# Kernel tuning notes

Measured on AMD Instinct MI355X. Metric: run time of the kernel, lower is better.

The kernel has to match this reference:

```python
import jax, jax.numpy as jnp
import numpy as np

N = 50000
E = 800000
F = 128


def gcn_smooth(edge_index, x):
    """Symmetric-normalized GCN smoothing: D^-1/2 (A + I) D^-1/2 x.

    edge_index: [2, E] int (src, dst) of a sparse graph; self-loops added here.
    x: [N, F] float node features.
    """
    src, dst = edge_index[0], edge_index[1]
    n = x.shape[0]
    # degree of A + I
    deg = jax.ops.segment_sum(jnp.ones((src.shape[0],), x.dtype), dst, num_segments=n) + 1.0
    dinv = jax.lax.rsqrt(deg)  # [N]
    # per-edge normalization d^-1/2[src] * d^-1/2[dst]
    norm_e = dinv[src] * dinv[dst]  # [E]
    msg = x[src] * norm_e[:, None]  # [E, F] -- gather + scale
    agg = jax.ops.segment_sum(msg, dst, num_segments=n)  # scatter-add over dst
    # self-loop contribution: dinv[i]^2 * x[i]
    return agg + (dinv * dinv)[:, None] * x


def setup_inputs() -> dict:
    key = jax.random.key(0)
    ks = jax.random.split(key, 12)
    inp = {
        "X_HypGNet": jax.random.normal(ks[0], (N, F), jnp.float32),
        "X_CGNet": jax.random.normal(ks[1], (N, F), jnp.float32),
        "X_SGNet": jax.random.normal(ks[2], (N, F), jnp.float32),
        "edge_index_hyp": jax.random.randint(ks[3], (2, E), 0, N, dtype=jnp.int32),
        "edge_index_c": jax.random.randint(ks[4], (2, E), 0, N, dtype=jnp.int32),
        "edge_index_s": jax.random.randint(ks[5], (2, E), 0, N, dtype=jnp.int32),
        "W_hyp": jax.random.normal(ks[6], (F, F), jnp.float32) * 0.05,
        "b_hyp": jax.random.normal(ks[7], (F,), jnp.float32) * 0.05,
        "W_cg": jax.random.normal(ks[8], (F, F), jnp.float32) * 0.05,
        "b_cg": jax.random.normal(ks[9], (F,), jnp.float32) * 0.05,
        "W_sg": jax.random.normal(ks[10], (F, F), jnp.float32) * 0.05,
        "b_sg": jax.random.normal(ks[11], (F,), jnp.float32) * 0.05,
    }
    return inp


def reference(X_HypGNet, X_CGNet, X_SGNet, edge_index_hyp, edge_index_c, edge_index_s,
              W_hyp, b_hyp, W_cg, b_cg, W_sg, b_sg):
    X_hyp = X_HypGNet @ W_hyp + b_hyp
    X_cg = X_CGNet @ W_cg + b_cg
    X_sg = X_SGNet @ W_sg + b_sg
    X_hyp_s = gcn_smooth(edge_index_hyp, X_hyp)
    X_cg_s = gcn_smooth(edge_index_c, X_cg)
    X_sg_s = gcn_smooth(edge_index_s, X_sg)
    return (X_hyp_s, X_cg_s, X_sg_s)
```

## Files before the change

### kernel.cpp

```cpp
#include <hip/hip_runtime.h>

#define F_DIM 128
#define NG 3
#define AEPT 16
#define CAP 48
#define MAXBIN 256
#define SPILL_CAP 8192

typedef __attribute__((ext_vector_type(8))) short short8_t;
typedef __attribute__((ext_vector_type(4))) float f32x4;

__device__ __forceinline__ unsigned short f2bf(float f) {
    unsigned int x = __float_as_uint(f);
    unsigned int r = x + 0x7fffu + ((x >> 16) & 1u);
    return (unsigned short)(r >> 16);
}
__device__ __forceinline__ float bflo(unsigned int u) { return __uint_as_float(u << 16); }
__device__ __forceinline__ float bfhi(unsigned int u) { return __uint_as_float(u & 0xffff0000u); }

struct GArgs {
    const int* src[NG]; const int* dst[NG];
    const float* X[NG]; const float* W[NG]; const float* b[NG];
    float* out[NG];
    unsigned short* Xps[NG];
    unsigned short* sorted[NG];
    int* binbuf[NG];
    int* bincur[NG];
    int* cstore[NG];
    float* dinv[NG];
    int* spill[NG];
    int* spill_n[NG];
    int nbin, bincap;
};

__global__ __launch_bounds__(256) void init_kernel(GArgs a, int g0) {
    int g = g0 + blockIdx.y;
    for (int i = threadIdx.x; i < a.nbin; i += 256) a.bincur[g][i] = i * a.bincap;
    if (threadIdx.x == 0) a.spill_n[g][0] = 0;
}

__global__ __launch_bounds__(256) void binA_kernel(GArgs a, int g0, int E) {
    int g = g0 + blockIdx.y;
    __shared__ int cnt[MAXBIN];
    __shared__ int lcur[MAXBIN];
    const int t = threadIdx.x;
    const int nbin = a.nbin, bincap = a.bincap;
    for (int i = t; i < nbin; i += 256) cnt[i] = 0;
    __syncthreads();
    const int* dst = a.dst[g];
    const int* src = a.src[g];
    const int base = blockIdx.x * (256 * AEPT) + t;
    int dd[AEPT], sv[AEPT];
#pragma unroll
    for (int i = 0; i < AEPT; ++i) {
        int e = base + i * 256;
        int ec = (e < E) ? e : 0;
        dd[i] = __builtin_nontemporal_load(&dst[ec]);
        sv[i] = __builtin_nontemporal_load(&src[ec]);
        if (e < E) atomicAdd(&cnt[dd[i] >> 8], 1);
    }
    __syncthreads();
    for (int i = t; i < nbin; i += 256) {
        int c = cnt[i];
        lcur[i] = c ? atomicAdd(&a.bincur[g][i], c) : 0;
    }
    __syncthreads();
    int* binbuf = a.binbuf[g];
#pragma unroll
    for (int i = 0; i < AEPT; ++i) {
        int e = base + i * 256;
        if (e < E) {
            int bin = dd[i] >> 8;
            int pos = atomicAdd(&lcur[bin], 1);
            if (pos < (bin + 1) * bincap) {
                binbuf[pos] = ((dd[i] & 255) << 16) | sv[i];
            } else {
                int sp = atomicAdd(a.spill_n[g], 1);
                if (sp < SPILL_CAP) {
                    a.spill[g][2 * sp] = sv[i];
                    a.spill[g][2 * sp + 1] = dd[i];
                }
            }
        }
    }
}

__global__ __launch_bounds__(256) void binB_kernel(GArgs a, int g0, int n) {
    int g = g0 + blockIdx.y;
    int bin = blockIdx.x;
    const int t = threadIdx.x;
    __shared__ int cnt[256];
    cnt[t] = 0;
    __syncthreads();
    const int bincap = a.bincap;
    int used = a.bincur[g][bin] - bin * bincap;
    int rd = min(used, bincap);
    const int* bb = a.binbuf[g] + bin * bincap;
    unsigned short* sorted = a.sorted[g];
    for (int j = t; j < rd; j += 256) {
        int u = bb[j];
        int dl = u >> 16;
        int s = u & 0xffff;
        int tk = atomicAdd(&cnt[dl], 1);
        int d = (bin << 8) + dl;
        if (tk < CAP) {
            sorted[d * CAP + tk] = (unsigned short)s;
        } else {
            int sp = atomicAdd(a.spill_n[g], 1);
            if (sp < SPILL_CAP) {
                a.spill[g][2 * sp] = s;
                a.spill[g][2 * sp + 1] = d;
            }
        }
    }
    __syncthreads();
    int d = (bin << 8) + t;
    if (d < n) {
        int deg = cnt[t];
        a.cstore[g][d] = min(deg, CAP);
        a.dinv[g][d] = rsqrtf((float)deg + 1.0f);
    }
}

__global__ __launch_bounds__(256) void gemm_kernel(GArgs a, int g0, int n) {
    int g = g0 + blockIdx.y;
    __shared__ unsigned short Xl[128 * 128];
    __shared__ unsigned short Wt[128 * 128];
    const int t = threadIdx.x;
    const int row0 = blockIdx.x * 128;
    const float* X = a.X[g];
    const float* W = a.W[g];
    char* XlB = (char*)Xl;
    char* WtB = (char*)Wt;

    for (int i = t; i < 128 * 16; i += 256) {
        int r = i >> 4, kc = i & 15;
        int row = row0 + r;
        float4 x0 = make_float4(0.f, 0.f, 0.f, 0.f), x1 = x0;
        if (row < n) {
            const float4* xp = (const float4*)(X + (size_t)row * F_DIM + kc * 8);
            x0 = xp[0]; x1 = xp[1];
        }
        uint4 pk;
        pk.x = (unsigned)f2bf(x0.x) | ((unsigned)f2bf(x0.y) << 16);
        pk.y = (unsigned)f2bf(x0.z) | ((unsigned)f2bf(x0.w) << 16);
        pk.z = (unsigned)f2bf(x1.x) | ((unsigned)f2bf(x1.y) << 16);
        pk.w = (unsigned)f2bf(x1.z) | ((unsigned)f2bf(x1.w) << 16);
        unsigned int ad = (unsigned)((r << 8) + (kc << 4)) ^ (unsigned)((r & 15) << 4);
        *(uint4*)(XlB + ad) = pk;
    }
    for (int i = t; i < 128 * 16; i += 256) {
        int nn = i & 127, kc = i >> 7;
        const float* wp = W + (size_t)(kc * 8) * F_DIM + nn;
        uint4 pk;
        pk.x = (unsigned)f2bf(wp[0])   | ((unsigned)f2bf(wp[128]) << 16);
        pk.y = (unsigned)f2bf(wp[256]) | ((unsigned)f2bf(wp[384]) << 16);
        pk.z = (unsigned)f2bf(wp[512]) | ((unsigned)f2bf(wp[640]) << 16);
        pk.w = (unsigned)f2bf(wp[768]) | ((unsigned)f2bf(wp[896]) << 16);
        unsigned int ad = (unsigned)((nn << 8) + (kc << 4)) ^ (unsigned)((nn & 15) << 4);
        *(uint4*)(WtB + ad) = pk;
    }
    __syncthreads();

    const int l = t & 63;
    const int wv = t >> 6;
    const int wr = wv >> 1, wc = wv & 1;
    const int lm = l & 15;
    const int lk = l >> 4;

    f32x4 acc[4][4] = {};
#pragma unroll
    for (int ks = 0; ks < 4; ++ks) {
        const int kb = ks * 64 + lk * 16;
        short8_t af[4], bv[4];
#pragma unroll
        for (int mt = 0; mt < 4; ++mt) {
            int r = wr * 64 + mt * 16 + lm;
            unsigned int ad = (unsigned)((r << 8) + kb) ^ (unsigned)((r & 15) << 4);
            af[mt] = *(const short8_t*)(XlB + ad);
        }
#pragma unroll
        for (int nt = 0; nt < 4; ++nt) {
            int c = wc * 64 + nt * 16 + lm;
            unsigned int ad = (unsigned)((c << 8) + kb) ^ (unsigned)((c & 15) << 4);
            bv[nt] = *(const short8_t*)(WtB + ad);
        }
#pragma unroll
        for (int mt = 0; mt < 4; ++mt)
#pragma unroll
            for (int nt = 0; nt < 4; ++nt)
                acc[mt][nt] = __builtin_amdgcn_mfma_f32_16x16x32_bf16(af[mt], bv[nt],
                                                                      acc[mt][nt], 0, 0, 0);
    }

    const float* bia = a.b[g];
    const float* dinv = a.dinv[g];
    unsigned short* Xps = a.Xps[g];
#pragma unroll
    for (int nt = 0; nt < 4; ++nt) {
        int col = wc * 64 + nt * 16 + lm;
        float bc = bia[col];
#pragma unroll
        for (int mt = 0; mt < 4; ++mt) {
            int rbase = row0 + wr * 64 + mt * 16 + lk * 4;
#pragma unroll
            for (int r = 0; r < 4; ++r) {
                int row = rbase + r;
                if (row < n) {
                    float v = (acc[mt][nt][r] + bc) * dinv[row];
                    Xps[(size_t)row * F_DIM + col] = f2bf(v);
                }
            }
        }
    }
}

__global__ __launch_bounds__(256) void agg_kernel(GArgs a, int g, int n) {
    int wave = (blockIdx.x * 256 + threadIdx.x) >> 6;
    if (wave >= n) return;
    const int l = threadIdx.x & 63;
    const int c = l & 15;
    const int hi = l >> 4;
    const uint4* Xp4 = (const uint4*)a.Xps[g];
    const unsigned short* sorted = a.sorted[g];
    int cnt = a.cstore[g][wave];
    int s = (l < cnt) ? (int)__builtin_nontemporal_load(&sorted[(size_t)wave * CAP + l]) : 0;
    float a0 = 0.f, a1 = 0.f, a2 = 0.f, a3 = 0.f, a4 = 0.f, a5 = 0.f, a6 = 0.f, a7 = 0.f;
    for (int k = 0; k < cnt; k += 8) {
        int e0 = k + hi, e1 = k + 4 + hi;
        int s0 = __shfl(s, e0, 64);
        int s1 = __shfl(s, e1 < 48 ? e1 : 0, 64);
        uint4 v0 = Xp4[(size_t)s0 * 16 + c];
        uint4 v1 = Xp4[(size_t)s1 * 16 + c];
        if (e0 >= cnt) v0 = make_uint4(0u, 0u, 0u, 0u);
        if (e1 >= cnt) v1 = make_uint4(0u, 0u, 0u, 0u);
        a0 += bflo(v0.x); a1 += bfhi(v0.x);
        a2 += bflo(v0.y); a3 += bfhi(v0.y);
        a4 += bflo(v0.z); a5 += bfhi(v0.z);
        a6 += bflo(v0.w); a7 += bfhi(v0.w);
        a0 += bflo(v1.x); a1 += bfhi(v1.x);
        a2 += bflo(v1.y); a3 += bfhi(v1.y);
        a4 += bflo(v1.z); a5 += bfhi(v1.z);
        a6 += bflo(v1.w); a7 += bfhi(v1.w);
    }
    a0 += __shfl_xor(a0, 16, 64); a0 += __shfl_xor(a0, 32, 64);
    a1 += __shfl_xor(a1, 16, 64); a1 += __shfl_xor(a1, 32, 64);
    a2 += __shfl_xor(a2, 16, 64); a2 += __shfl_xor(a2, 32, 64);
    a3 += __shfl_xor(a3, 16, 64); a3 += __shfl_xor(a3, 32, 64);
    a4 += __shfl_xor(a4, 16, 64); a4 += __shfl_xor(a4, 32, 64);
    a5 += __shfl_xor(a5, 16, 64); a5 += __shfl_xor(a5, 32, 64);
    a6 += __shfl_xor(a6, 16, 64); a6 += __shfl_xor(a6, 32, 64);
    a7 += __shfl_xor(a7, 16, 64); a7 += __shfl_xor(a7, 32, 64);
    uint4 v = Xp4[(size_t)wave * 16 + c];
    a0 += bflo(v.x); a1 += bfhi(v.x);
    a2 += bflo(v.y); a3 += bfhi(v.y);
    a4 += bflo(v.z); a5 += bfhi(v.z);
    a6 += bflo(v.w); a7 += bfhi(v.w);
    float dd = a.dinv[g][wave];
    if (hi == 0) {
        float* o = (float*)a.out[g] + (size_t)wave * F_DIM + c * 8;
        *(float4*)(o + 0) = make_float4(a0 * dd, a1 * dd, a2 * dd, a3 * dd);
        *(float4*)(o + 4) = make_float4(a4 * dd, a5 * dd, a6 * dd, a7 * dd);
    }
}

__global__ __launch_bounds__(128) void spill_kernel(GArgs a, int g0) {
    int g = g0 + blockIdx.y;
    int ns = min(a.spill_n[g][0], SPILL_CAP);
    const unsigned short* Xps = a.Xps[g];
    const float* dinv = a.dinv[g];
    float* out = a.out[g];
    for (int i = blockIdx.x; i < ns; i += gridDim.x) {
        int s = a.spill[g][2 * i];
        int d = a.spill[g][2 * i + 1];
        float w = dinv[d];
        int f = threadIdx.x;
        float v = __uint_as_float(((unsigned int)Xps[(size_t)s * F_DIM + f]) << 16);
        unsafeAtomicAdd(&out[(size_t)d * F_DIM + f], w * v);
    }
}

extern "C" void kernel_launch(void* const* d_in, const int* in_sizes, int n_in,
                              void* d_out, int out_size, void* d_ws, size_t ws_size,
                              hipStream_t stream) {
    const float* Xin[NG] = {(const float*)d_in[0], (const float*)d_in[1], (const float*)d_in[2]};
    const int* ei[NG] = {(const int*)d_in[3], (const int*)d_in[4], (const int*)d_in[5]};
    const float* Wk[NG] = {(const float*)d_in[6], (const float*)d_in[8], (const float*)d_in[10]};
    const float* bk[NG] = {(const float*)d_in[7], (const float*)d_in[9], (const float*)d_in[11]};

    const int N = in_sizes[0] / F_DIM;
    const int E = in_sizes[3] / 2;
    float* out = (float*)d_out;

    const int nbin = (N + 255) >> 8;
    const int bincap = E / nbin + E / (3 * nbin) + 256;

    const size_t xps_b = (size_t)N * F_DIM * 2;
    const size_t sorted_b = (size_t)N * CAP * 2;
    const size_t binbuf_b = (size_t)nbin * bincap * 4;
    const size_t nb = (size_t)N * 4;
    const size_t bincur_b = ((size_t)nbin * 4 + 255) / 256 * 256;
    const size_t spill_b = (size_t)SPILL_CAP * 8 + 64;
    const size_t per = ((xps_b + sorted_b + binbuf_b + 2 * nb + bincur_b + spill_b + 255)
                        / 256) * 256;
    const bool fused = ws_size >= (size_t)NG * per;
    char* base = (char*)d_ws;

    GArgs a;
    a.nbin = nbin;
    a.bincap = bincap;
    for (int r = 0; r < NG; ++r) {
        char* s = base + (size_t)(fused ? r : 0) * per;
        size_t off = 0;
        a.Xps[r] = (unsigned short*)(s + off); off += xps_b;
        a.sorted[r] = (unsigned short*)(s + off); off += sorted_b;
        a.binbuf[r] = (int*)(s + off); off += binbuf_b;
        a.cstore[r] = (int*)(s + off); off += nb;
        a.dinv[r] = (float*)(s + off); off += nb;
        a.bincur[r] = (int*)(s + off); off += bincur_b;
        a.spill[r] = (int*)(s + off);
        a.spill_n[r] = (int*)(s + off + spill_b - 64);
        a.src[r] = ei[r];
        a.dst[r] = ei[r] + E;
        a.X[r] = Xin[r];
        a.W[r] = Wk[r];
        a.b[r] = bk[r];
        a.out[r] = out + (size_t)r * N * F_DIM;
    }

    const dim3 blk(256);
    const int gAe = (E + 256 * AEPT - 1) / (256 * AEPT);
    const int gR = (N + 127) / 128;
    const int gG = (N * 64 + 255) / 256;

    if (fused) {
        init_kernel<<<dim3(1, NG), blk, 0, stream>>>(a, 0);
        binA_kernel<<<dim3(gAe, NG), blk, 0, stream>>>(a, 0, E);
        binB_kernel<<<dim3(nbin, NG), blk, 0, stream>>>(a, 0, N);
        gemm_kernel<<<dim3(gR, NG), blk, 0, stream>>>(a, 0, N);
        for (int g = 0; g < NG; ++g)
            agg_kernel<<<dim3(gG, 1), blk, 0, stream>>>(a, g, N);
        spill_kernel<<<dim3(16, NG), dim3(128), 0, stream>>>(a, 0);
    } else {
        for (int g = 0; g < NG; ++g) {
            init_kernel<<<dim3(1, 1), blk, 0, stream>>>(a, g);
            binA_kernel<<<dim3(gAe, 1), blk, 0, stream>>>(a, g, E);
            binB_kernel<<<dim3(nbin, 1), blk, 0, stream>>>(a, g, N);
            gemm_kernel<<<dim3(gR, 1), blk, 0, stream>>>(a, g, N);
            agg_kernel<<<dim3(gG, 1), blk, 0, stream>>>(a, g, N);
            spill_kernel<<<dim3(16, 1), dim3(128), 0, stream>>>(a, g);
        }
    }
}
```

Before: 201.6 us.

## Pre-convert weights once and load GEMM operands directly into registers

A new small kernel converts each W to bf16 in MFMA fragment layout once per graph. The GEMM then drops its LDS staging and barrier, loading X rows straight from global memory into registers and converting them to bf16 in place. The three per-graph aggregation launches are merged into one launch indexed by blockIdx.y. This removes per-block redundant W conversion, LDS traffic and launch overhead, but X loads are no longer coalesced through shared memory and an extra kernel launch is added.

After: 193.0 us. -4.3%, faster.

```diff
diff --git a/kernel.cpp b/kernel.cpp
--- a/kernel.cpp
+++ b/kernel.cpp
@@ -18,12 +18,22 @@
 __device__ __forceinline__ float bflo(unsigned int u) { return __uint_as_float(u << 16); }
 __device__ __forceinline__ float bfhi(unsigned int u) { return __uint_as_float(u & 0xffff0000u); }
 
+__device__ __forceinline__ short8_t cvt8(float4 x0, float4 x1) {
+    union { short8_t s; uint4 u; } pk;
+    pk.u.x = (unsigned)f2bf(x0.x) | ((unsigned)f2bf(x0.y) << 16);
+    pk.u.y = (unsigned)f2bf(x0.z) | ((unsigned)f2bf(x0.w) << 16);
+    pk.u.z = (unsigned)f2bf(x1.x) | ((unsigned)f2bf(x1.y) << 16);
+    pk.u.w = (unsigned)f2bf(x1.z) | ((unsigned)f2bf(x1.w) << 16);
+    return pk.s;
+}
+
 struct GArgs {
     const int* src[NG]; const int* dst[NG];
     const float* X[NG]; const float* W[NG]; const float* b[NG];
     float* out[NG];
     unsigned short* Xps[NG];
     unsigned short* sorted[NG];
+    unsigned short* Wtb[NG];
     int* binbuf[NG];
     int* bincur[NG];
     int* cstore[NG];
@@ -37,6 +47,22 @@
     int g = g0 + blockIdx.y;
     for (int i = threadIdx.x; i < a.nbin; i += 256) a.bincur[g][i] = i * a.bincap;
     if (threadIdx.x == 0) a.spill_n[g][0] = 0;
+}
+
+__global__ __launch_bounds__(256) void prew_kernel(GArgs a, int g0) {
+    int g = g0 + blockIdx.y;
+    const float* W = a.W[g];
+    unsigned short* Wtb = a.Wtb[g];
+    for (int i = threadIdx.x; i < 16 * 128; i += 256) {
+        int kg = i >> 7, c = i & 127;
+        const float* wp = W + (size_t)(kg * 8) * F_DIM + c;
+        uint4 pk;
+        pk.x = (unsigned)f2bf(wp[0])   | ((unsigned)f2bf(wp[128]) << 16);
+        pk.y = (unsigned)f2bf(wp[256]) | ((unsigned)f2bf(wp[384]) << 16);
+        pk.z = (unsigned)f2bf(wp[512]) | ((unsigned)f2bf(wp[640]) << 16);
+        pk.w = (unsigned)f2bf(wp[768]) | ((unsigned)f2bf(wp[896]) << 16);
+        *(uint4*)(Wtb + (size_t)i * 8) = pk;
+    }
 }
 
 __global__ __launch_bounds__(256) void binA_kernel(GArgs a, int g0, int E) {
@@ -124,85 +150,54 @@
 
 __global__ __launch_bounds__(256) void gemm_kernel(GArgs a, int g0, int n) {
     int g = g0 + blockIdx.y;
-    __shared__ unsigned short Xl[128 * 128];
-    __shared__ unsigned short Wt[128 * 128];
     const int t = threadIdx.x;
-    const int row0 = blockIdx.x * 128;
-    const float* X = a.X[g];
-    const float* W = a.W[g];
-    char* XlB = (char*)Xl;
-    char* WtB = (char*)Wt;
-
-    for (int i = t; i < 128 * 16; i += 256) {
-        int r = i >> 4, kc = i & 15;
-        int row = row0 + r;
-        float4 x0 = make_float4(0.f, 0.f, 0.f, 0.f), x1 = x0;
-        if (row < n) {
-            const float4* xp = (const float4*)(X + (size_t)row * F_DIM + kc * 8);
-            x0 = xp[0]; x1 = xp[1];
-        }
-        uint4 pk;
-        pk.x = (unsigned)f2bf(x0.x) | ((unsigned)f2bf(x0.y) << 16);
-        pk.y = (unsigned)f2bf(x0.z) | ((unsigned)f2bf(x0.w) << 16);
-        pk.z = (unsigned)f2bf(x1.x) | ((unsigned)f2bf(x1.y) << 16);
-        pk.w = (unsigned)f2bf(x1.z) | ((unsigned)f2bf(x1.w) << 16);
-        unsigned int ad = (unsigned)((r << 8) + (kc << 4)) ^ (unsigned)((r & 15) << 4);
-        *(uint4*)(XlB + ad) = pk;
-    }
-    for (int i = t; i < 128 * 16; i += 256) {
-        int nn = i & 127, kc = i >> 7;
-        const float* wp = W + (size_t)(kc * 8) * F_DIM + nn;
-        uint4 pk;
-        pk.x = (unsigned)f2bf(wp[0])   | ((unsigned)f2bf(wp[128]) << 16);
-        pk.y = (unsigned)f2bf(wp[256]) | ((unsigned)f2bf(wp[384]) << 16);
-        pk.z = (unsigned)f2bf(wp[512]) | ((unsigned)f2bf(wp[640]) << 16);
-        pk.w = (unsigned)f2bf(wp[768]) | ((unsigned)f2bf(wp[896]) << 16);
-        unsigned int ad = (unsigned)((nn << 8) + (kc << 4)) ^ (unsigned)((nn & 15) << 4);
-        *(uint4*)(WtB + ad) = pk;
-    }
-    __syncthreads();
-
     const int l = t & 63;
     const int wv = t >> 6;
     const int wr = wv >> 1, wc = wv & 1;
-    const int lm = l & 15;
-    const int lk = l >> 4;
+    const int lm = l & 15, lk = l >> 4;
+    const int rowA = blockIdx.x * 128 + wr * 64 + lm;
+    const float* X = a.X[g];
+    const unsigned short* Wtb = a.Wtb[g];
 
     f32x4 acc[4][4] = {};
 #pragma unroll
     for (int ks = 0; ks < 4; ++ks) {
-        const int kb = ks * 64 + lk * 16;
-        short8_t af[4], bv[4];
+        short8_t bv[4];
+#pragma unroll
+        for (int nt = 0; nt < 4; ++nt) {
+            int col = wc * 64 + nt * 16 + lm;
+            bv[nt] = *(const short8_t*)(Wtb + ((size_t)((ks * 4 + lk) * 128 + col)) * 8);
+        }
+        float4 xr[4][2];
 #pragma unroll
         for (int mt = 0; mt < 4; ++mt) {
-            int r = wr * 64 + mt * 16 + lm;
-            unsigned int ad = (unsigned)((r << 8) + kb) ^ (unsigned)((r & 15) << 4);
-            af[mt] = *(const short8_t*)(XlB + ad);
-        }
-#pragma unroll
-        for (int nt = 0; nt < 4; ++nt) {
-            int c = wc * 64 + nt * 16 + lm;
-            unsigned int ad = (unsigned)((c << 8) + kb) ^ (unsigned)((c & 15) << 4);
-            bv[nt] = *(const short8_t*)(WtB + ad);
-        }
-#pragma unroll
-        for (int mt = 0; mt < 4; ++mt)
+            int row = rowA + mt * 16;
+            row = row < n ? row : n - 1;
+            const float4* xp = (const float4*)(X + (size_t)row * F_DIM + ks * 32 + lk * 8);
+            xr[mt][0] = xp[0];
+            xr[mt][1] = xp[1];
+        }
+#pragma unroll
+        for (int mt = 0; mt < 4; ++mt) {
+            short8_t af = cvt8(xr[mt][0], xr[mt][1]);
 #pragma unroll
             for (int nt = 0; nt < 4; ++nt)
-                acc[mt][nt] = __builtin_amdgcn_mfma_f32_16x16x32_bf16(af[mt], bv[nt],
+                acc[mt][nt] = __builtin_amdgcn_mfma_f32_16x16x32_bf16(af, bv[nt],
                                                                       acc[mt][nt], 0, 0, 0);
+        }
     }
 
     const float* bia = a.b[g];
     const float* dinv = a.dinv[g];
     unsigned short* Xps = a.Xps[g];
+    const int rb = blockIdx.x * 128 + wr * 64;
 #pragma unroll
     for (int nt = 0; nt < 4; ++nt) {
         int col = wc * 64 + nt * 16 + lm;
         float bc = bia[col];
 #pragma unroll
         for (int mt = 0; mt < 4; ++mt) {
-            int rbase = row0 + wr * 64 + mt * 16 + lk * 4;
+            int rbase = rb + mt * 16 + lk * 4;
 #pragma unroll
             for (int r = 0; r < 4; ++r) {
                 int row = rbase + r;
@@ -215,7 +210,8 @@
     }
 }
 
-__global__ __launch_bounds__(256) void agg_kernel(GArgs a, int g, int n) {
+__global__ __launch_bounds__(256) void agg_kernel(GArgs a, int g0, int n) {
+    int g = g0 + blockIdx.y;
     int wave = (blockIdx.x * 256 + threadIdx.x) >> 6;
     if (wave >= n) return;
     const int l = threadIdx.x & 63;
@@ -229,7 +225,7 @@
     for (int k = 0; k < cnt; k += 8) {
         int e0 = k + hi, e1 = k + 4 + hi;
         int s0 = __shfl(s, e0, 64);
-        int s1 = __shfl(s, e1 < 48 ? e1 : 0, 64);
+        int s1 = __shfl(s, e1 < CAP ? e1 : 0, 64);
         uint4 v0 = Xp4[(size_t)s0 * 16 + c];
         uint4 v1 = Xp4[(size_t)s1 * 16 + c];
         if (e0 >= cnt) v0 = make_uint4(0u, 0u, 0u, 0u);
@@ -297,12 +293,13 @@
 
     const size_t xps_b = (size_t)N * F_DIM * 2;
     const size_t sorted_b = (size_t)N * CAP * 2;
+    const size_t wtb_b = (size_t)16 * 128 * 8 * 2;
     const size_t binbuf_b = (size_t)nbin * bincap * 4;
     const size_t nb = (size_t)N * 4;
     const size_t bincur_b = ((size_t)nbin * 4 + 255) / 256 * 256;
     const size_t spill_b = (size_t)SPILL_CAP * 8 + 64;
-    const size_t per = ((xps_b + sorted_b + binbuf_b + 2 * nb + bincur_b + spill_b + 255)
-                        / 256) * 256;
+    const size_t per = ((xps_b + sorted_b + wtb_b + binbuf_b + 2 * nb + bincur_b + spill_b
+                         + 255) / 256) * 256;
     const bool fused = ws_size >= (size_t)NG * per;
     char* base = (char*)d_ws;
 
@@ -314,6 +311,7 @@
         size_t off = 0;
         a.Xps[r] = (unsigned short*)(s + off); off += xps_b;
         a.sorted[r] = (unsigned short*)(s + off); off += sorted_b;
+        a.Wtb[r] = (unsigned short*)(s + off); off += wtb_b;
         a.binbuf[r] = (int*)(s + off); off += binbuf_b;
         a.cstore[r] = (int*)(s + off); off += nb;
         a.dinv[r] = (float*)(s + off); off += nb;
@@ -335,15 +333,16 @@
 
     if (fused) {
         init_kernel<<<dim3(1, NG), blk, 0, stream>>>(a, 0);
+        prew_kernel<<<dim3(1, NG), blk, 0, stream>>>(a, 0);
         binA_kernel<<<dim3(gAe, NG), blk, 0, stream>>>(a, 0, E);
         binB_kernel<<<dim3(nbin, NG), blk, 0, stream>>>(a, 0, N);
         gemm_kernel<<<dim3(gR, NG), blk, 0, stream>>>(a, 0, N);
-        for (int g = 0; g < NG; ++g)
-            agg_kernel<<<dim3(gG, 1), blk, 0, stream>>>(a, g, N);
+        agg_kernel<<<dim3(gG, NG), blk, 0, stream>>>(a, 0, N);
         spill_kernel<<<dim3(16, NG), dim3(128), 0, stream>>>(a, 0);
     } else {
         for (int g = 0; g < NG; ++g) {
             init_kernel<<<dim3(1, 1), blk, 0, stream>>>(a, g);
+            prew_kernel<<<dim3(1, 1), blk, 0, stream>>>(a, g);
             binA_kernel<<<dim3(gAe, 1), blk, 0, stream>>>(a, g, E);
             binB_kernel<<<dim3(nbin, 1), blk, 0, stream>>>(a, g, N);
             gemm_kernel<<<dim3(gR, 1), blk, 0, stream>>>(a, g, N);
```
